# Kernel tuning notes

Hardware: AMD Instinct MI355X
Metric: run time of the kernel (lower is better)

The kernel has to match this reference:

```python
import jax, jax.numpy as jnp
import numpy as np

# Config (matches init_kwargs defaults): V=25 joints, C=16 -> D=400, heads=2,
# ffn=64*25=1600, window L=9, stride=1, postnorm, gelu, dropout ignored (eval).
N, C, T, V = 16, 16, 300, 25
D = C * V          # 400
H = 2              # nhead
FF = 64 * V        # 1600
L = 9              # trans_length
MAX_LEN = 301


def _layernorm(x, g, b, eps=1e-5):
    mu = jnp.mean(x, axis=-1, keepdims=True)
    var = jnp.mean(jnp.square(x - mu), axis=-1, keepdims=True)
    return (x - mu) * jax.lax.rsqrt(var + eps) * g + b


def setup_inputs() -> dict:
    key = jax.random.key(0)
    ks = jax.random.split(key, 12)
    s = 0.02
    return {
        "x": jax.random.normal(ks[0], (N, C, T, V), jnp.float32),
        "pe": jax.random.normal(ks[1], (1, MAX_LEN, D), jnp.float32) * s,
        "w_in": jax.random.normal(ks[2], (3 * D, D), jnp.float32) * s,
        "b_in": jnp.zeros((3 * D,), jnp.float32),
        "w_out": jax.random.normal(ks[3], (D, D), jnp.float32) * s,
        "b_out": jnp.zeros((D,), jnp.float32),
        "w1": jax.random.normal(ks[4], (FF, D), jnp.float32) * s,
        "b1": jnp.zeros((FF,), jnp.float32),
        "w2": jax.random.normal(ks[5], (D, FF), jnp.float32) * s,
        "b2": jnp.zeros((D,), jnp.float32),
        "ln1_g": jnp.ones((D,), jnp.float32),
        "ln1_b": jnp.zeros((D,), jnp.float32),
        "ln2_g": jnp.ones((D,), jnp.float32),
        "ln2_b": jnp.zeros((D,), jnp.float32),
    }


def _encoder_layer(h, w_in, b_in, w_out, b_out, w1, b1, w2, b2,
                   ln1_g, ln1_b, ln2_g, ln2_b):
    # h: [B, L, D]; post-norm TransformerEncoderLayer (torch default)
    B, Lw, Dm = h.shape
    dh = Dm // H
    qkv = h @ w_in.T + b_in                             # [B,L,3D]
    q, k, v = jnp.split(qkv, 3, axis=-1)
    def heads(t):
        return t.reshape(B, Lw, H, dh).transpose(0, 2, 1, 3)  # [B,H,L,dh]
    q, k, v = heads(q), heads(k), heads(v)
    scores = jnp.einsum('bhqd,bhkd->bhqk', q, k) / np.float32(np.sqrt(dh))
    att = jax.nn.softmax(scores, axis=-1)
    o = jnp.einsum('bhqk,bhkd->bhqd', att, v)
    o = o.transpose(0, 2, 1, 3).reshape(B, Lw, Dm) @ w_out.T + b_out
    h = _layernorm(h + o, ln1_g, ln1_b)
    ff = jax.nn.gelu(h @ w1.T + b1, approximate=False) @ w2.T + b2
    return _layernorm(h + ff, ln2_g, ln2_b)


def reference(x, pe, w_in, b_in, w_out, b_out, w1, b1, w2, b2,
              ln1_g, ln1_b, ln2_g, ln2_b):
    n, c, t, v = x.shape
    d = c * v
    # [N,C,T,V] -> [N,T,V,C] -> [N,T,D]  (flatten order is (V,C), as in torch view)
    xs = x.transpose(0, 2, 3, 1).reshape(n, t, d)
    xs = xs + pe[:, :t, :]
    W = t - L                                            # number of windows (stride=1)
    win = jnp.arange(W)
    idx = win[:, None] + jnp.arange(L)[None, :]          # [W,L] gather indices
    xw = xs[:, idx, :].reshape(n * W, L, d)              # batched windows
    out = _encoder_layer(xw, w_in, b_in, w_out, b_out, w1, b1, w2, b2,
                         ln1_g, ln1_b, ln2_g, ln2_b)
    out = out.reshape(n, W * L, d)
    # window i writes into rows i//2 : i//2 + L and results are summed
    pos = ((win // 2)[:, None] + jnp.arange(L)[None, :]).reshape(-1)  # [W*L]
    xt = jnp.zeros((n, t, d), xs.dtype).at[:, pos, :].add(out)
    # [N,T,D] -> [N,T,V,C] -> [N,C,T,V]
    return xt.reshape(n, t, v, c).transpose(0, 3, 1, 2)
```

## Files before the change

### kernel.cpp

```cpp
#include <hip/hip_runtime.h>
#include <cstdint>
#include <cstddef>

#define N_    16
#define C_    16
#define T_    300
#define V_    25
#define D_    400
#define H_    2
#define DH_   200
#define FF_   1600
#define L_    9
#define W_    291
#define NW_   (N_*W_)
#define NT_   (N_*T_)

#define KP_   416
#define SD_   400
#define SQKV_ 1200
#define SFF_  1600

#define WIN_OFF   0u
#define WOUT_OFF  1064960u
#define W1_OFF    1490944u
#define W2_OFF    2875392u
#define XS_OFF    4513792u
#define QKV_OFF   8404992u
#define ACC_OFF   20078592u
#define HEAD_END  27758592u

#define WAIT_VM4   0xF74
#define WAIT_VM0   0xF70

using u16 = unsigned short;
using u32 = unsigned int;
using frag  = __attribute__((ext_vector_type(8))) short;
using f32x4 = __attribute__((ext_vector_type(4))) float;

__device__ __forceinline__ float bf2f(u16 u){
  return __uint_as_float(((u32)u) << 16);
}
__device__ __forceinline__ u16 f2bf(float f){
  return (u16)((__float_as_uint(f) + 0x8000u) >> 16);
}
__device__ __forceinline__ float gelu_f(float v){
  float v2  = v * v;
  float u   = v * (0.7978845608f + 0.03567740814f * v2);
  float u2  = u * u;
  float num = u * (27.f + u2);
  float den = 27.f + 9.f * u2;
  float th  = num * __builtin_amdgcn_rcpf(den);
  th = fminf(fmaxf(th, -1.f), 1.f);
  return 0.5f * v * (1.f + th);
}
__device__ __forceinline__ void unpack8(uint4 v, float* o){
  o[0] = bf2f((u16)(v.x & 0xffffu)); o[1] = bf2f((u16)(v.x >> 16));
  o[2] = bf2f((u16)(v.y & 0xffffu)); o[3] = bf2f((u16)(v.y >> 16));
  o[4] = bf2f((u16)(v.z & 0xffffu)); o[5] = bf2f((u16)(v.z >> 16));
  o[6] = bf2f((u16)(v.w & 0xffffu)); o[7] = bf2f((u16)(v.w >> 16));
}

__device__ __forceinline__ void convw_body(const float* src, u16* dst,
                                           int dN, int dK, int sN, int sK, int idx){
  if (idx >= dN * dK) return;
  int n = idx / dK, k = idx % dK;
  dst[idx] = (n < sN && k < sK) ? f2bf(src[(size_t)n * sK + k]) : (u16)0;
}

#define PREP_GRID 23816
__global__ __launch_bounds__(256) void prep_kernel(const float* __restrict__ x,
                                                   const float* __restrict__ pe,
                                                   const float* __restrict__ w_in,
                                                   const float* __restrict__ w_out,
                                                   const float* __restrict__ w1,
                                                   const float* __restrict__ w2,
                                                   u16* __restrict__ xs,
                                                   u16* __restrict__ w_in_b,
                                                   u16* __restrict__ w_out_b,
                                                   u16* __restrict__ w1_b,
                                                   u16* __restrict__ w2_b,
                                                   float* __restrict__ acc){
  int b = blockIdx.x;
  int tid = threadIdx.x;
  if (b < 7500){
    int idx = b * 256 + tid;
    if (idx < NT_ * D_) acc[idx] = 0.f;
  } else if (b < 15000){
    int idx = (b - 7500) * 256 + tid;
    if (idx < NT_ * D_){
      int d  = idx % D_;
      int nt = idx / D_;
      int t  = nt % T_;
      int n  = nt / T_;
      float val = x[(((size_t)(n*C_ + (d & 15)))*T_ + t)*V_ + (d >> 4)] + pe[t*D_ + d];
      xs[idx] = f2bf(val);
    }
  } else if (b < 17080){
    convw_body(w_in,  w_in_b,  1280, KP_, 1200, D_,  (b - 15000) * 256 + tid);
  } else if (b < 17912){
    convw_body(w_out, w_out_b,  512, KP_,  400, D_,  (b - 17080) * 256 + tid);
  } else if (b < 20616){
    convw_body(w1,    w1_b,   1664, KP_, 1600, D_,  (b - 17912) * 256 + tid);
  } else {
    convw_body(w2,    w2_b,    512, SFF_, 400, FF_, (b - 20616) * 256 + tid);
  }
}

template<int ACT>
__global__ __launch_bounds__(256) void gemm_mfma(const u16* __restrict__ A, int lda,
                                                 const u16* __restrict__ B, int ldb,
                                                 const float* __restrict__ bias,
                                                 u16* __restrict__ C, int ldc,
                                                 int Nn, int KPd,
                                                 int gx, int gy){
  __shared__ u16 smem[24576];
  int id = blockIdx.x;
  int c  = id & 7, t = id >> 3;
  int bx = t % gx;
  int by = (t / gx) * 8 + c;
  if (by >= gy) return;
  const int m0 = by * 128, n0 = bx * 128;

  const int tid  = threadIdx.x;
  const int lane = tid & 63;
  const int wv   = tid >> 6;
  const int quad = lane >> 4, l16 = lane & 15;
  const int wm   = wv & 1,   wn  = wv >> 1;

  const int rl   = lane >> 2;
  const int sseg = (lane & 3) ^ ((lane >> 3) & 3);
  const u16* Ag = A + (size_t)(m0 + wv*32 + rl) * lda + sseg*8;
  const u16* Bg = B + (size_t)(n0 + wv*32 + rl) * ldb + sseg*8;

  f32x4 acc[4][4] = {};
  const int sa = quad ^ ((l16 >> 1) & 3);

  auto stage = [&](int buf, int kt){
    u16* Ad = &smem[buf*4096 + (wv*32)*32];
    u16* Bd = &smem[12288 + buf*4096 + (wv*32)*32];
    #pragma unroll
    for (int h = 0; h < 2; ++h){
      __builtin_amdgcn_global_load_lds(
          (const __attribute__((address_space(1))) void*)(Ag + kt + (size_t)(16*h)*lda),
          (__attribute__((address_space(3))) void*)(Ad + h*16*32), 16, 0, 0);
      __builtin_amdgcn_global_load_lds(
          (const __attribute__((address_space(1))) void*)(Bg + kt + (size_t)(16*h)*ldb),
          (__attribute__((address_space(3))) void*)(Bd + h*16*32), 16, 0, 0);
    }
  };

  const int nit = KPd >> 5;
  stage(0, 0);
  stage(1, 32);
  int nb = 2;
  for (int it = 0; it < nit; ++it){
    if (it < nit - 1) __builtin_amdgcn_s_waitcnt(WAIT_VM4);
    else              __builtin_amdgcn_s_waitcnt(WAIT_VM0);
    __builtin_amdgcn_s_barrier();
    if (it + 2 < nit){
      stage(nb, (it + 2) << 5);
      nb = (nb == 2) ? 0 : nb + 1;
    }
    const int buf = it % 3;
    const u16* Ar = &smem[buf*4096];
    const u16* Br = &smem[12288 + buf*4096];
    frag af[4], bfr[4];
    #pragma unroll
    for (int i = 0; i < 4; ++i){
      af[i]  = *(const frag*)(&Ar[(wm*64 + i*16 + l16)*32 + sa*8]);
      bfr[i] = *(const frag*)(&Br[(wn*64 + i*16 + l16)*32 + sa*8]);
    }
    #pragma unroll
    for (int i = 0; i < 4; ++i)
      #pragma unroll
      for (int j = 0; j < 4; ++j)
        acc[i][j] = __builtin_amdgcn_mfma_f32_16x16x32_bf16(af[i], bfr[j], acc[i][j], 0, 0, 0);
  }

  __builtin_amdgcn_s_barrier();

  u16* ep = &smem[wv * 4608];
  #pragma unroll
  for (int j = 0; j < 4; ++j){
    int n = n0 + wn*64 + j*16 + l16;
    float bj = (n < Nn) ? bias[n] : 0.f;
    #pragma unroll
    for (int i = 0; i < 4; ++i){
      #pragma unroll
      for (int r = 0; r < 4; ++r){
        float v = acc[i][j][r] + bj;
        if (ACT) v = gelu_f(v);
        ep[(i*16 + quad*4 + r)*72 + j*16 + l16] = f2bf(v);
      }
    }
  }
  #pragma unroll
  for (int p = 0; p < 8; ++p){
    int row = p*8 + (lane >> 3);
    int seg = lane & 7;
    int nc  = n0 + wn*64 + seg*8;
    if (nc < Nn){
      uint4 v = *(const uint4*)(&ep[row*72 + seg*8]);
      *(uint4*)(C + (size_t)(m0 + wm*64 + row)*ldc + nc) = v;
    }
  }
}

__global__ __launch_bounds__(256) void attn_kernel(const u16* __restrict__ qkv,
                                                   u16* __restrict__ o,
                                                   int g0){
  __shared__ float sq[L_ * 1200];
  __shared__ float sc[H_ * L_ * L_];
  __shared__ float att[H_ * L_ * L_];
  const int g = g0 + blockIdx.x;
  const int n = g / W_, w = g % W_;
  const int tid = threadIdx.x;

  for (int i = tid; i < L_ * 150; i += 256){
    int l = i / 150, ck = i % 150;
    uint4 v = *(const uint4*)(qkv + ((size_t)(n*T_ + w + l)) * SQKV_ + ck*8);
    unpack8(v, &sq[l*1200 + ck*8]);
  }
  __syncthreads();

  if (tid < H_ * L_ * L_){
    int h = tid / (L_*L_), rem = tid % (L_*L_), qi = rem / L_, ki = rem % L_;
    const float* qp = &sq[qi*1200 + h*DH_];
    const float* kp = &sq[ki*1200 + D_ + h*DH_];
    float s = 0.f;
    for (int dd = 0; dd < DH_; ++dd) s += qp[dd] * kp[dd];
    sc[tid] = s * 0.07071067811865475f;
  }
  __syncthreads();

  if (tid < H_ * L_){
    int base = tid * L_;
    float mx = -1e30f;
    for (int j = 0; j < L_; ++j) mx = fmaxf(mx, sc[base + j]);
    float sum = 0.f;
    for (int j = 0; j < L_; ++j){ float e = __expf(sc[base + j] - mx); att[base + j] = e; sum += e; }
    float inv = 1.f / sum;
    for (int j = 0; j < L_; ++j) att[base + j] *= inv;
  }
  __syncthreads();

  for (int i = tid; i < L_ * D_; i += 256){
    int l = i / D_, d = i % D_;
    int h = d / DH_;
    float a = 0.f;
    #pragma unroll
    for (int ki = 0; ki < L_; ++ki)
      a += att[h*(L_*L_) + l*L_ + ki] * sq[ki*1200 + 2*D_ + d];
    o[((size_t)blockIdx.x * L_ + l) * SD_ + d] = f2bf(a);
  }
}

__global__ __launch_bounds__(256) void ln1_kernel(const u16* __restrict__ y,
                                                  const float* __restrict__ gam,
                                                  const float* __restrict__ bet,
                                                  u16* __restrict__ out,
                                                  const u16* __restrict__ xs,
                                                  int g0){
  const int wv = threadIdx.x >> 6, lane = threadIdx.x & 63;
  const int r = blockIdx.x * 4 + wv;
  const int g = g0 + r / L_, l = r % L_;
  const int n = g / W_, w = g % W_;
  const u16* arow = xs + ((size_t)(n*T_ + w + l)) * SD_;
  const u16* brow = y + (size_t)r * SD_;

  const bool act = lane < 50;
  float v[8];
  float s = 0.f, s2 = 0.f;
  if (act){
    float a8[8], b8[8];
    unpack8(*(const uint4*)(arow + lane*8), a8);
    unpack8(*(const uint4*)(brow + lane*8), b8);
    #pragma unroll
    for (int i = 0; i < 8; ++i){ v[i] = a8[i] + b8[i]; s += v[i]; s2 += v[i]*v[i]; }
  } else {
    #pragma unroll
    for (int i = 0; i < 8; ++i) v[i] = 0.f;
  }
  #pragma unroll
  for (int off = 32; off; off >>= 1){
    s  += __shfl_xor(s,  off);
    s2 += __shfl_xor(s2, off);
  }
  float mean = s * (1.f / D_);
  float rstd = rsqrtf(s2 * (1.f / D_) - mean*mean + 1e-5f);
  if (act){
    float4 ga = *(const float4*)(gam + lane*8);
    float4 gb = *(const float4*)(gam + lane*8 + 4);
    float4 ba = *(const float4*)(bet + lane*8);
    float4 bb = *(const float4*)(bet + lane*8 + 4);
    float gg[8] = {ga.x,ga.y,ga.z,ga.w, gb.x,gb.y,gb.z,gb.w};
    float bb8[8]= {ba.x,ba.y,ba.z,ba.w, bb.x,bb.y,bb.z,bb.w};
    u32 o4[4];
    #pragma unroll
    for (int i = 0; i < 4; ++i){
      u16 lo = f2bf((v[2*i]   - mean) * rstd * gg[2*i]   + bb8[2*i]);
      u16 hi = f2bf((v[2*i+1] - mean) * rstd * gg[2*i+1] + bb8[2*i+1]);
      o4[i] = (u32)lo | ((u32)hi << 16);
    }
    *(uint4*)(out + (size_t)r * SD_ + lane*8) = make_uint4(o4[0],o4[1],o4[2],o4[3]);
  }
}

__global__ __launch_bounds__(256) void ln2_scatter_kernel(const u16* __restrict__ h,
                                                          const u16* __restrict__ y,
                                                          const float* __restrict__ gam,
                                                          const float* __restrict__ bet,
                                                          float* __restrict__ acc,
                                                          int g0){
  __shared__ float buf[4][400];
  const int wv = threadIdx.x >> 6, lane = threadIdx.x & 63;
  const int tid = threadIdx.x;
  const int r0 = blockIdx.x * 4;
  {
    const int r = r0 + wv;
    const u16* arow = h + (size_t)r * SD_;
    const u16* brow = y + (size_t)r * SD_;
    const bool act = lane < 50;
    float v[8];
    float s = 0.f, s2 = 0.f;
    if (act){
      float a8[8], b8[8];
      unpack8(*(const uint4*)(arow + lane*8), a8);
      unpack8(*(const uint4*)(brow + lane*8), b8);
      #pragma unroll
      for (int i = 0; i < 8; ++i){ v[i] = a8[i] + b8[i]; s += v[i]; s2 += v[i]*v[i]; }
    } else {
      #pragma unroll
      for (int i = 0; i < 8; ++i) v[i] = 0.f;
    }
    #pragma unroll
    for (int off = 32; off; off >>= 1){
      s  += __shfl_xor(s,  off);
      s2 += __shfl_xor(s2, off);
    }
    float mean = s * (1.f / D_);
    float rstd = rsqrtf(s2 * (1.f / D_) - mean*mean + 1e-5f);
    if (act){
      float4 ga = *(const float4*)(gam + lane*8);
      float4 gb = *(const float4*)(gam + lane*8 + 4);
      float4 ba = *(const float4*)(bet + lane*8);
      float4 bb = *(const float4*)(bet + lane*8 + 4);
      float gg[8] = {ga.x,ga.y,ga.z,ga.w, gb.x,gb.y,gb.z,gb.w};
      float bb8[8]= {ba.x,ba.y,ba.z,ba.w, bb.x,bb.y,bb.z,bb.w};
      #pragma unroll
      for (int i = 0; i < 8; ++i)
        buf[wv][lane*8 + i] = (v[i] - mean) * rstd * gg[i] + bb8[i];
    }
  }
  __syncthreads();
  #pragma unroll
  for (int rr = 0; rr < 4; ++rr){
    int r = r0 + rr;
    int g = g0 + r / L_, l = r % L_;
    int n = g / W_, w = g % W_;
    size_t base = ((size_t)(n*T_ + (w >> 1) + l)) * D_;
    atomicAdd(acc + base + tid, buf[rr][tid]);
    if (tid + 256 < D_) atomicAdd(acc + base + tid + 256, buf[rr][tid + 256]);
  }
}

__global__ __launch_bounds__(256) void final_kernel(const float* __restrict__ acc,
                                                    float* __restrict__ dout){
  int idx = blockIdx.x * 256 + threadIdx.x;
  if (idx >= NT_ * D_) return;
  int d  = idx % D_;
  int nt = idx / D_;
  int t  = nt % T_;
  int n  = nt / T_;
  dout[(((size_t)(n*C_ + (d & 15)))*T_ + t)*V_ + (d >> 4)] = acc[idx];
}

extern "C" void kernel_launch(void* const* d_in, const int* in_sizes, int n_in,
                              void* d_out, int out_size, void* d_ws, size_t ws_size,
                              hipStream_t stream){
  (void)in_sizes; (void)n_in; (void)out_size;
  const float* x     = (const float*)d_in[0];
  const float* pe    = (const float*)d_in[1];
  const float* w_in  = (const float*)d_in[2];
  const float* b_in  = (const float*)d_in[3];
  const float* w_out = (const float*)d_in[4];
  const float* b_out = (const float*)d_in[5];
  const float* w1    = (const float*)d_in[6];
  const float* b1    = (const float*)d_in[7];
  const float* w2    = (const float*)d_in[8];
  const float* b2    = (const float*)d_in[9];
  const float* ln1g  = (const float*)d_in[10];
  const float* ln1b  = (const float*)d_in[11];
  const float* ln2g  = (const float*)d_in[12];
  const float* ln2b  = (const float*)d_in[13];

  int nch = 3;
  {
    size_t need1 = (size_t)HEAD_END + (size_t)41984 * 5600;
    size_t need2 = (size_t)HEAD_END + (size_t)20992 * 5600;
    if (ws_size >= need1 + (1u<<20)) nch = 1;
    else if (ws_size >= need2 + (1u<<20)) nch = 2;
  }
  const int CW  = NW_ / nch;
  const int RC  = CW * L_;
  const int RCP = ((RC + 127) / 128) * 128;

  char* ws = (char*)d_ws;
  u16*   w_in_b  = (u16*)(ws + WIN_OFF);
  u16*   w_out_b = (u16*)(ws + WOUT_OFF);
  u16*   w1_b    = (u16*)(ws + W1_OFF);
  u16*   w2_b    = (u16*)(ws + W2_OFF);
  u16*   xs      = (u16*)(ws + XS_OFF);
  u16*   qkv     = (u16*)(ws + QKV_OFF);
  float* acc     = (float*)(ws + ACC_OFF);
  u16*   o_c     = (u16*)(ws + HEAD_END);
  u16*   y_c     = o_c + (size_t)RCP * SD_;
  u16*   h_c     = y_c + (size_t)RCP * SD_;
  u16*   ffc     = h_c + (size_t)RCP * SD_;

  prep_kernel<<<PREP_GRID, 256, 0, stream>>>(x, pe, w_in, w_out, w1, w2,
                                             xs, w_in_b, w_out_b, w1_b, w2_b, acc);

  {
    int gx = 10, gy = (NT_ + 127)/128, gy8 = (gy + 7) & ~7;
    gemm_mfma<0><<<gx*gy8, 256, 0, stream>>>(
        xs, SD_, w_in_b, KP_, b_in, qkv, SQKV_, 1200, KP_, gx, gy);
  }

  const int gyc = RCP/128, gyc8 = (gyc + 7) & ~7;

  for (int g0 = 0; g0 < NW_; g0 += CW){
    attn_kernel<<<CW, 256, 0, stream>>>(qkv, o_c, g0);

    gemm_mfma<0><<<4*gyc8, 256, 0, stream>>>(
        o_c, SD_, w_out_b, KP_, b_out, y_c, SD_, D_, KP_, 4, gyc);

    ln1_kernel<<<RC/4, 256, 0, stream>>>(y_c, ln1g, ln1b, h_c, xs, g0);

    gemm_mfma<1><<<13*gyc8, 256, 0, stream>>>(
        h_c, SD_, w1_b, KP_, b1, ffc, SFF_, FF_, KP_, 13, gyc);

    gemm_mfma<0><<<4*gyc8, 256, 0, stream>>>(
        ffc, SFF_, w2_b, SFF_, b2, y_c, SD_, D_, SFF_, 4, gyc);

    ln2_scatter_kernel<<<RC/4, 256, 0, stream>>>(h_c, y_c, ln2g, ln2b, acc, g0);
  }

  final_kernel<<<(NT_*D_ + 255)/256, 256, 0, stream>>>(acc, (float*)d_out);
}
```

Baseline: 437.7 us.

## Batch eight windows per attention block sharing K/V rows via LDS

The attention kernel now gives each block 8 consecutive windows. It loads the 16 shared token rows of bf16 QKV straight into LDS once with global_load_lds, instead of reloading and unpacking 9 rows per window into fp32. Score and PV computation read packed bf16 with vectorized loads, and outputs are written as 4-wide packed stores. The grid covers all windows of all batches, so each chunk iteration launches blocks that early-exit or mask outside the chunk range. That adds idle launched blocks and more index arithmetic.

```diff
diff --git a/kernel.cpp b/kernel.cpp
--- a/kernel.cpp
+++ b/kernel.cpp
@@ -206,52 +206,93 @@
   }
 }
 
+#define WB_     8
+#define ATT_NB  37
+#define ATT_GRID (N_ * ATT_NB)
 __global__ __launch_bounds__(256) void attn_kernel(const u16* __restrict__ qkv,
                                                    u16* __restrict__ o,
-                                                   int g0){
-  __shared__ float sq[L_ * 1200];
-  __shared__ float sc[H_ * L_ * L_];
-  __shared__ float att[H_ * L_ * L_];
-  const int g = g0 + blockIdx.x;
-  const int n = g / W_, w = g % W_;
-  const int tid = threadIdx.x;
-
-  for (int i = tid; i < L_ * 150; i += 256){
-    int l = i / 150, ck = i % 150;
-    uint4 v = *(const uint4*)(qkv + ((size_t)(n*T_ + w + l)) * SQKV_ + ck*8);
-    unpack8(v, &sq[l*1200 + ck*8]);
-  }
+                                                   int g0, int gend){
+  __shared__ u16 kv[20480];
+  __shared__ float att[WB_ * 2 * 81];
+  const int b  = blockIdx.x;
+  const int n  = b / ATT_NB;
+  const int w0 = (b - n * ATT_NB) * WB_;
+  const int gbase = n * W_ + w0;
+  if (gbase >= gend || gbase + WB_ <= g0) return;
+
+  const int tid  = threadIdx.x;
+  const int lane = tid & 63;
+  const int wv   = tid >> 6;
+
+  const char* gsrc = (const char*)(qkv + (size_t)(n * T_ + w0) * SQKV_);
+  #pragma unroll
+  for (int j = 0; j < 10; ++j){
+    __builtin_amdgcn_global_load_lds(
+        (const __attribute__((address_space(1))) void*)(gsrc + j*4096 + wv*1024 + lane*16),
+        (__attribute__((address_space(3))) void*)((char*)kv + j*4096 + wv*1024),
+        16, 0, 0);
+  }
+  __builtin_amdgcn_s_waitcnt(WAIT_VM0);
   __syncthreads();
 
-  if (tid < H_ * L_ * L_){
-    int h = tid / (L_*L_), rem = tid % (L_*L_), qi = rem / L_, ki = rem % L_;
-    const float* qp = &sq[qi*1200 + h*DH_];
-    const float* kp = &sq[ki*1200 + D_ + h*DH_];
+  for (int i = tid; i < WB_ * 162; i += 256){
+    int w  = i / 162;
+    int r  = i - w * 162;
+    int h  = r / 81;
+    int p  = r - h * 81;
+    int qi = p / 9, ki = p - qi * 9;
+    const u16* qp = kv + (w + qi) * 1200 + h * DH_;
+    const u16* kp = kv + (w + ki) * 1200 + D_ + h * DH_;
     float s = 0.f;
-    for (int dd = 0; dd < DH_; ++dd) s += qp[dd] * kp[dd];
-    sc[tid] = s * 0.07071067811865475f;
+    #pragma unroll 5
+    for (int cch = 0; cch < 25; ++cch){
+      float qa[8], kb[8];
+      unpack8(*(const uint4*)(qp + cch*8), qa);
+      unpack8(*(const uint4*)(kp + cch*8), kb);
+      #pragma unroll
+      for (int e = 0; e < 8; ++e) s += qa[e] * kb[e];
+    }
+    att[i] = s * 0.07071067811865475f;
   }
   __syncthreads();
 
-  if (tid < H_ * L_){
-    int base = tid * L_;
-    float mx = -1e30f;
-    for (int j = 0; j < L_; ++j) mx = fmaxf(mx, sc[base + j]);
-    float sum = 0.f;
-    for (int j = 0; j < L_; ++j){ float e = __expf(sc[base + j] - mx); att[base + j] = e; sum += e; }
+  if (tid < WB_ * 18){
+    float* row = att + tid * 9;
+    float mx = row[0];
+    #pragma unroll
+    for (int j = 1; j < 9; ++j) mx = fmaxf(mx, row[j]);
+    float e[9]; float sum = 0.f;
+    #pragma unroll
+    for (int j = 0; j < 9; ++j){ e[j] = __expf(row[j] - mx); sum += e[j]; }
     float inv = 1.f / sum;
-    for (int j = 0; j < L_; ++j) att[base + j] *= inv;
+    #pragma unroll
+    for (int j = 0; j < 9; ++j) row[j] = e[j] * inv;
   }
   __syncthreads();
 
-  for (int i = tid; i < L_ * D_; i += 256){
-    int l = i / D_, d = i % D_;
-    int h = d / DH_;
-    float a = 0.f;
-    #pragma unroll
-    for (int ki = 0; ki < L_; ++ki)
-      a += att[h*(L_*L_) + l*L_ + ki] * sq[ki*1200 + 2*D_ + d];
-    o[((size_t)blockIdx.x * L_ + l) * SD_ + d] = f2bf(a);
+  for (int i = tid; i < WB_ * 900; i += 256){
+    int w  = i / 900;
+    int r  = i - w * 900;
+    int l  = r / 100;
+    int c4 = r - l * 100;
+    int h  = (c4 >= 50) ? 1 : 0;
+    const float* ap = att + (w*2 + h)*81 + l*9;
+    float o4[4] = {0.f, 0.f, 0.f, 0.f};
+    #pragma unroll
+    for (int ki = 0; ki < 9; ++ki){
+      float a = ap[ki];
+      uint2 vv = *(const uint2*)(kv + (w + ki)*1200 + 2*D_ + c4*4);
+      o4[0] += a * bf2f((u16)(vv.x & 0xffffu));
+      o4[1] += a * bf2f((u16)(vv.x >> 16));
+      o4[2] += a * bf2f((u16)(vv.y & 0xffffu));
+      o4[3] += a * bf2f((u16)(vv.y >> 16));
+    }
+    int g = gbase + w;
+    if (w0 + w < W_ && g >= g0 && g < gend){
+      u32 lo = (u32)f2bf(o4[0]) | ((u32)f2bf(o4[1]) << 16);
+      u32 hi = (u32)f2bf(o4[2]) | ((u32)f2bf(o4[3]) << 16);
+      *(uint2*)(o + ((size_t)(g - g0) * L_ + l) * SD_ + c4*4) = make_uint2(lo, hi);
+    }
   }
 }
 
@@ -430,7 +471,7 @@
   const int gyc = RCP/128, gyc8 = (gyc + 7) & ~7;
 
   for (int g0 = 0; g0 < NW_; g0 += CW){
-    attn_kernel<<<CW, 256, 0, stream>>>(qkv, o_c, g0);
+    attn_kernel<<<ATT_GRID, 256, 0, stream>>>(qkv, o_c, g0, g0 + CW);
 
     gemm_mfma<0><<<4*gyc8, 256, 0, stream>>>(
         o_c, SD_, w_out_b, KP_, b_out, y_c, SD_, D_, KP_, 4, gyc);
```

New measurement: 431.6 us. About the same (-1.4%).
